# Kernel optimization log

Hardware: AMD Instinct MI355X
Metric: run time of the kernel (lower is better)

The kernel has to match this reference:

```python
import jax, jax.numpy as jnp
import numpy as np

WINDOW = 5
PAD = WINDOW // 2


def _extract_patches(x):
    # x: (B,C,H,W) -> patches (B,C,K*K,H,W) with reflect padding, matching
    # F.pad(mode='reflect') + F.unfold(window, padding=0).
    B, C, H, W = x.shape
    xp = jnp.pad(x, ((0, 0), (0, 0), (PAD, PAD), (PAD, PAD)), mode='reflect')
    patches = jnp.stack(
        [xp[:, :, i:i + H, j:j + W] for i in range(WINDOW) for j in range(WINDOW)],
        axis=2,
    )
    return patches


def setup_inputs() -> dict:
    key = jax.random.key(0)
    k1, k2, k3 = jax.random.split(key, 3)
    x = jax.random.normal(k1, (4, 32, 256, 256), dtype=jnp.float32)
    mix = jax.random.normal(k2, (1, 32, 1, 1), dtype=jnp.float32)
    beta_raw = jax.random.normal(k3, (), dtype=jnp.float32)
    return {"x": x, "mix": mix, "beta_raw": beta_raw}


def reference(x, mix, beta_raw):
    patches = _extract_patches(x)  # (B,C,25,H,W)

    # Max filter (= max_pool2d over reflect-padded input, stride 1)
    max_out = jnp.max(patches, axis=2)

    # Soft (differentiable) median filter
    beta = 5.0 + 45.0 * jax.nn.sigmoid(beta_raw)
    center = jnp.mean(patches, axis=2, keepdims=True)
    weights = jax.nn.softmax(-beta * jnp.abs(patches - center), axis=2)
    median_out = jnp.sum(weights * patches, axis=2)

    lambda_c = jax.nn.sigmoid(mix)  # (1,C,1,1)
    return lambda_c * median_out + (1.0 - lambda_c) * max_out
```

## Files before the change

### kernel.cpp

```cpp
#include <hip/hip_runtime.h>
#include <math.h>

#define HW 256
#define TW 64
#define TH 32
#define LW 68
#define LH 36

typedef float f32x2 __attribute__((ext_vector_type(2)));

__device__ __forceinline__ int reflect_idx(int i) {
    i = (i < 0) ? -i : i;
    i = (i >= HW) ? (2 * HW - 2 - i) : i;
    return i;
}

__device__ __forceinline__ float4 max4(float4 a, float4 b) {
    float4 r; r.x = fmaxf(a.x, b.x); r.y = fmaxf(a.y, b.y);
    r.z = fmaxf(a.z, b.z); r.w = fmaxf(a.w, b.w); return r;
}
__device__ __forceinline__ float4 max34(float4 a, float4 b, float4 c) {
    float4 r; r.x = fmaxf(fmaxf(a.x, b.x), c.x); r.y = fmaxf(fmaxf(a.y, b.y), c.y);
    r.z = fmaxf(fmaxf(a.z, b.z), c.z); r.w = fmaxf(fmaxf(a.w, b.w), c.w); return r;
}
__device__ __forceinline__ float4 add4(float4 a, float4 b) {
    float4 r; r.x = a.x + b.x; r.y = a.y + b.y;
    r.z = a.z + b.z; r.w = a.w + b.w; return r;
}
__device__ __forceinline__ float4 sub4(float4 a, float4 b) {
    float4 r; r.x = a.x - b.x; r.y = a.y - b.y;
    r.z = a.z - b.z; r.w = a.w - b.w; return r;
}

__device__ __forceinline__ void proc_row(
    float4 A0, float4 B0, float4 A1, float4 B1, float4 A2, float4 B2,
    float4 A3, float4 B3, float4 A4, float4 B4,
    float4 cmA, float4 cmB, float4 csA, float4 csB,
    float bp, float c04b, float inv_bp, float lam,
    float* __restrict__ orow)
{
    const float cs[8] = {csA.x,csA.y,csA.z,csA.w, csB.x,csB.y,csB.z,csB.w};
    const float cm[8] = {cmA.x,cmA.y,cmA.z,cmA.w, cmB.x,cmB.y,cmB.z,cmB.w};
    const float vv[5][8] = {
        {A0.x,A0.y,A0.z,A0.w, B0.x,B0.y,B0.z,B0.w},
        {A1.x,A1.y,A1.z,A1.w, B1.x,B1.y,B1.z,B1.w},
        {A2.x,A2.y,A2.z,A2.w, B2.x,B2.y,B2.z,B2.w},
        {A3.x,A3.y,A3.z,A3.w, B3.x,B3.y,B3.z,B3.w},
        {A4.x,A4.y,A4.z,A4.w, B4.x,B4.y,B4.z,B4.w}};

    const float t12 = cs[1] + cs[2];
    const float t34 = cs[3] + cs[4];
    const float t56 = cs[5] + cs[6];
    const float u   = t12 + t34;
    const float w_  = t34 + t56;
    const float S[4] = {cs[0] + u, u + cs[5], cs[2] + w_, w_ + cs[7]};

    const float h12 = fmaxf(cm[1], cm[2]);
    const float h34 = fmaxf(cm[3], cm[4]);
    const float h56 = fmaxf(cm[5], cm[6]);
    const float m[4] = {fmaxf(fmaxf(cm[0], h12), h34),
                        fmaxf(fmaxf(h12, h34), cm[5]),
                        fmaxf(fmaxf(cm[2], h34), h56),
                        fmaxf(fmaxf(h34, h56), cm[7])};

    const f32x2 bp2   = {bp, bp};
    const f32x2 nbm01 = {-(S[0] * c04b), -(S[1] * c04b)};
    const f32x2 nbm23 = {-(S[2] * c04b), -(S[3] * c04b)};
    f32x2 ws01 = {0.0f, 0.0f}, ws23 = {0.0f, 0.0f};
    f32x2 wa01 = {0.0f, 0.0f}, wa23 = {0.0f, 0.0f};

    #pragma unroll
    for (int k = 0; k < 5; ++k) {
        #pragma unroll
        for (int j = 0; j < 5; ++j) {
            const f32x2 v01 = {vv[k][j],     vv[k][j + 1]};
            const f32x2 v23 = {vv[k][j + 2], vv[k][j + 3]};
            const f32x2 tv01 = __builtin_elementwise_fma(bp2, v01, nbm01);
            const f32x2 tv23 = __builtin_elementwise_fma(bp2, v23, nbm23);
            f32x2 e01, e23;
            e01.x = __builtin_amdgcn_exp2f(-fabsf(tv01.x));
            e01.y = __builtin_amdgcn_exp2f(-fabsf(tv01.y));
            e23.x = __builtin_amdgcn_exp2f(-fabsf(tv23.x));
            e23.y = __builtin_amdgcn_exp2f(-fabsf(tv23.y));
            ws01 += e01;
            ws23 += e23;
            wa01 = __builtin_elementwise_fma(e01, tv01, wa01);
            wa23 = __builtin_elementwise_fma(e23, tv23, wa23);
        }
    }

    const float ws[4] = {ws01.x, ws01.y, ws23.x, ws23.y};
    const float wa[4] = {wa01.x, wa01.y, wa23.x, wa23.y};

    float o[4];
    #pragma unroll
    for (int p = 0; p < 4; ++p) {
        const float mean = S[p] * 0.04f;
        const float med  = fmaf(wa[p] * __builtin_amdgcn_rcpf(ws[p]), inv_bp, mean);
        o[p] = fmaf(lam, med - m[p], m[p]);
    }
    float4 o4; o4.x = o[0]; o4.y = o[1]; o4.z = o[2]; o4.w = o[3];
    *(float4*)orow = o4;
}

__global__ __launch_bounds__(256, 4)
void maxmedian_kernel(const float* __restrict__ x,
                      const float* __restrict__ mix,
                      const float* __restrict__ beta_raw,
                      float* __restrict__ out,
                      int C) {
    __shared__ __align__(16) float tile[LH * LW];

    const int tiles_x = HW / TW;
    const int tiles_per_plane = tiles_x * (HW / TH);
    const int plane = blockIdx.x / tiles_per_plane;
    const int t     = blockIdx.x % tiles_per_plane;
    const int ty0 = (t / tiles_x) * TH;
    const int tx0 = (t % tiles_x) * TW;

    const float* __restrict__ xp = x + (size_t)plane * (HW * HW);
    const int tid = threadIdx.x;

    {
        const int c   = tid & 63;
        const int r0s = tid >> 6;
        const int gx  = tx0 + c;
        #pragma unroll
        for (int k = 0; k < 9; ++k) {
            const int r  = r0s + 4 * k;
            const int gy = reflect_idx(ty0 + r - 2);
            tile[r * LW + c + 2] = xp[gy * HW + gx];
        }
        if (tid < 144) {
            const int jj = tid & 3;
            const int j  = (jj < 2) ? jj : (64 + jj);
            const int r  = tid >> 2;
            const int gx2 = reflect_idx(tx0 + j - 2);
            const int gy2 = reflect_idx(ty0 + r - 2);
            tile[r * LW + j] = xp[gy2 * HW + gx2];
        }
    }
    __syncthreads();

    const int ch = plane % C;
    const float lam  = 1.0f / (1.0f + __expf(-mix[ch]));
    const float beta = 5.0f + 45.0f / (1.0f + __expf(-beta_raw[0]));
    const float bp     = beta * 1.44269504088896f;
    const float inv_bp = 1.0f / bp;
    const float c04b   = 0.04f * bp;

    const int tx  = tid & 15;
    const int ryq = tid >> 4;
    const int r0  = ryq * 2;
    const float* lbase = &tile[r0 * LW + 4 * tx];

    float4 w0a = *(const float4*)(lbase + 0 * LW);
    float4 w0b = *(const float4*)(lbase + 0 * LW + 4);
    float4 w1a = *(const float4*)(lbase + 1 * LW);
    float4 w1b = *(const float4*)(lbase + 1 * LW + 4);
    float4 w2a = *(const float4*)(lbase + 2 * LW);
    float4 w2b = *(const float4*)(lbase + 2 * LW + 4);
    float4 w3a = *(const float4*)(lbase + 3 * LW);
    float4 w3b = *(const float4*)(lbase + 3 * LW + 4);
    float4 w4a = *(const float4*)(lbase + 4 * LW);
    float4 w4b = *(const float4*)(lbase + 4 * LW + 4);
    float4 w5a = *(const float4*)(lbase + 5 * LW);
    float4 w5b = *(const float4*)(lbase + 5 * LW + 4);

    float4 csA = add4(add4(add4(w0a, w1a), add4(w2a, w3a)), w4a);
    float4 csB = add4(add4(add4(w0b, w1b), add4(w2b, w3b)), w4b);

    const float4 p12a = max4(w1a, w2a), p12b = max4(w1b, w2b);
    const float4 p34a = max4(w3a, w4a), p34b = max4(w3b, w4b);
    const float4 cm0a = max34(w0a, p12a, p34a);
    const float4 cm0b = max34(w0b, p12b, p34b);

    float* __restrict__ orow =
        out + (size_t)plane * (HW * HW) + (size_t)(ty0 + r0) * HW + (tx0 + 4 * tx);

    proc_row(w0a,w0b, w1a,w1b, w2a,w2b, w3a,w3b, w4a,w4b,
             cm0a, cm0b, csA, csB, bp, c04b, inv_bp, lam, orow);

    csA = add4(csA, sub4(w5a, w0a));
    csB = add4(csB, sub4(w5b, w0b));
    const float4 cm1a = max34(p12a, p34a, w5a);
    const float4 cm1b = max34(p12b, p34b, w5b);

    proc_row(w1a,w1b, w2a,w2b, w3a,w3b, w4a,w4b, w5a,w5b,
             cm1a, cm1b, csA, csB, bp, c04b, inv_bp, lam, orow + HW);
}

extern "C" void kernel_launch(void* const* d_in, const int* in_sizes, int n_in,
                              void* d_out, int out_size, void* d_ws, size_t ws_size,
                              hipStream_t stream) {
    const float* x        = (const float*)d_in[0];
    const float* mix      = (const float*)d_in[1];
    const float* beta_raw = (const float*)d_in[2];
    float* out            = (float*)d_out;

    const int planes = in_sizes[0] / (HW * HW);
    const int C      = in_sizes[1];
    const int tiles_per_plane = (HW / TW) * (HW / TH);
    const int grid = planes * tiles_per_plane;

    maxmedian_kernel<<<grid, 256, 0, stream>>>(x, mix, beta_raw, out, C);
}
```

Before: 39.33 us.

## Restructure into per-wave bands with double-buffered LDS software pipeline

Each wave now owns an 8-row band of one plane and walks four 64-column tiles. It prefetches the next tile's rows into registers while computing the current tile out of a double-buffered per-wave LDS region, and syncs with wave barriers only instead of block-wide __syncthreads. The aim is to overlap global load latency with the exp-heavy compute and to drop block synchronisation. In exchange the grid shrinks to planes*8 blocks (1024), halo rows are reloaded per 8-row band (12 loaded rows for 8 output rows, against 36 for 32 before), and register pressure rises from the staged tiles, with the occupancy hint removed.

```diff
diff --git a/kernel.cpp b/kernel.cpp
--- a/kernel.cpp
+++ b/kernel.cpp
@@ -2,10 +2,9 @@
 #include <math.h>
 
 #define HW 256
-#define TW 64
-#define TH 32
 #define LW 68
-#define LH 36
+#define WLH 12
+#define NT 4
 
 typedef float f32x2 __attribute__((ext_vector_type(2)));
 
@@ -31,6 +30,11 @@
     float4 r; r.x = a.x - b.x; r.y = a.y - b.y;
     r.z = a.z - b.z; r.w = a.w - b.w; return r;
 }
+
+struct Stage {
+    float m[WLH];
+    float h;
+};
 
 __device__ __forceinline__ void proc_row(
     float4 A0, float4 B0, float4 A1, float4 B1, float4 A2, float4 B2,
@@ -103,44 +107,32 @@
     *(float4*)orow = o4;
 }
 
-__global__ __launch_bounds__(256, 4)
+__global__ __launch_bounds__(256)
 void maxmedian_kernel(const float* __restrict__ x,
                       const float* __restrict__ mix,
                       const float* __restrict__ beta_raw,
                       float* __restrict__ out,
                       int C) {
-    __shared__ __align__(16) float tile[LH * LW];
-
-    const int tiles_x = HW / TW;
-    const int tiles_per_plane = tiles_x * (HW / TH);
-    const int plane = blockIdx.x / tiles_per_plane;
-    const int t     = blockIdx.x % tiles_per_plane;
-    const int ty0 = (t / tiles_x) * TH;
-    const int tx0 = (t % tiles_x) * TW;
+    __shared__ __align__(16) float lds[4][2][WLH * LW];
+
+    const int tid  = threadIdx.x;
+    const int wave = tid >> 6;
+    const int lane = tid & 63;
+
+    const int band  = blockIdx.x * 4 + wave;
+    const int plane = band >> 5;
+    const int by0   = (band & 31) << 3;
 
     const float* __restrict__ xp = x + (size_t)plane * (HW * HW);
-    const int tid = threadIdx.x;
-
-    {
-        const int c   = tid & 63;
-        const int r0s = tid >> 6;
-        const int gx  = tx0 + c;
-        #pragma unroll
-        for (int k = 0; k < 9; ++k) {
-            const int r  = r0s + 4 * k;
-            const int gy = reflect_idx(ty0 + r - 2);
-            tile[r * LW + c + 2] = xp[gy * HW + gx];
-        }
-        if (tid < 144) {
-            const int jj = tid & 3;
-            const int j  = (jj < 2) ? jj : (64 + jj);
-            const int r  = tid >> 2;
-            const int gx2 = reflect_idx(tx0 + j - 2);
-            const int gy2 = reflect_idx(ty0 + r - 2);
-            tile[r * LW + j] = xp[gy2 * HW + gx2];
-        }
-    }
-    __syncthreads();
+
+    int gy[WLH];
+    #pragma unroll
+    for (int k = 0; k < WLH; ++k) gy[k] = reflect_idx(by0 - 2 + k) * HW;
+
+    const int hj   = lane & 3;
+    const int hcol = (hj < 2) ? hj : (64 + hj);
+    const int hoff = hcol - 2;
+    const int gyh  = reflect_idx(by0 - 2 + (lane >> 2)) * HW;
 
     const int ch = plane % C;
     const float lam  = 1.0f / (1.0f + __expf(-mix[ch]));
@@ -149,45 +141,87 @@
     const float inv_bp = 1.0f / bp;
     const float c04b   = 0.04f * bp;
 
-    const int tx  = tid & 15;
-    const int ryq = tid >> 4;
-    const int r0  = ryq * 2;
-    const float* lbase = &tile[r0 * LW + 4 * tx];
-
-    float4 w0a = *(const float4*)(lbase + 0 * LW);
-    float4 w0b = *(const float4*)(lbase + 0 * LW + 4);
-    float4 w1a = *(const float4*)(lbase + 1 * LW);
-    float4 w1b = *(const float4*)(lbase + 1 * LW + 4);
-    float4 w2a = *(const float4*)(lbase + 2 * LW);
-    float4 w2b = *(const float4*)(lbase + 2 * LW + 4);
-    float4 w3a = *(const float4*)(lbase + 3 * LW);
-    float4 w3b = *(const float4*)(lbase + 3 * LW + 4);
-    float4 w4a = *(const float4*)(lbase + 4 * LW);
-    float4 w4b = *(const float4*)(lbase + 4 * LW + 4);
-    float4 w5a = *(const float4*)(lbase + 5 * LW);
-    float4 w5b = *(const float4*)(lbase + 5 * LW + 4);
-
-    float4 csA = add4(add4(add4(w0a, w1a), add4(w2a, w3a)), w4a);
-    float4 csB = add4(add4(add4(w0b, w1b), add4(w2b, w3b)), w4b);
-
-    const float4 p12a = max4(w1a, w2a), p12b = max4(w1b, w2b);
-    const float4 p34a = max4(w3a, w4a), p34b = max4(w3b, w4b);
-    const float4 cm0a = max34(w0a, p12a, p34a);
-    const float4 cm0b = max34(w0b, p12b, p34b);
-
-    float* __restrict__ orow =
-        out + (size_t)plane * (HW * HW) + (size_t)(ty0 + r0) * HW + (tx0 + 4 * tx);
-
-    proc_row(w0a,w0b, w1a,w1b, w2a,w2b, w3a,w3b, w4a,w4b,
-             cm0a, cm0b, csA, csB, bp, c04b, inv_bp, lam, orow);
-
-    csA = add4(csA, sub4(w5a, w0a));
-    csB = add4(csB, sub4(w5b, w0b));
-    const float4 cm1a = max34(p12a, p34a, w5a);
-    const float4 cm1b = max34(p12b, p34b, w5b);
-
-    proc_row(w1a,w1b, w2a,w2b, w3a,w3b, w4a,w4b, w5a,w5b,
-             cm1a, cm1b, csA, csB, bp, c04b, inv_bp, lam, orow + HW);
+    const int tx = lane & 15;
+    const int r0 = (lane >> 4) * 2;
+
+    auto stage_load = [&](int t, Stage& s) {
+        const int c0 = t * 64;
+        #pragma unroll
+        for (int k = 0; k < WLH; ++k)
+            s.m[k] = xp[gy[k] + c0 + lane];
+        if (lane < 48)
+            s.h = xp[gyh + reflect_idx(c0 + hoff)];
+    };
+    auto stage_write = [&](int buf, const Stage& s) {
+        float* __restrict__ b = lds[wave][buf];
+        #pragma unroll
+        for (int k = 0; k < WLH; ++k)
+            b[k * LW + 2 + lane] = s.m[k];
+        if (lane < 48)
+            b[(lane >> 2) * LW + hcol] = s.h;
+    };
+    auto compute = [&](int t, int buf) {
+        const float* lbase = &lds[wave][buf][r0 * LW + 4 * tx];
+
+        float4 w0a = *(const float4*)(lbase + 0 * LW);
+        float4 w0b = *(const float4*)(lbase + 0 * LW + 4);
+        float4 w1a = *(const float4*)(lbase + 1 * LW);
+        float4 w1b = *(const float4*)(lbase + 1 * LW + 4);
+        float4 w2a = *(const float4*)(lbase + 2 * LW);
+        float4 w2b = *(const float4*)(lbase + 2 * LW + 4);
+        float4 w3a = *(const float4*)(lbase + 3 * LW);
+        float4 w3b = *(const float4*)(lbase + 3 * LW + 4);
+        float4 w4a = *(const float4*)(lbase + 4 * LW);
+        float4 w4b = *(const float4*)(lbase + 4 * LW + 4);
+        float4 w5a = *(const float4*)(lbase + 5 * LW);
+        float4 w5b = *(const float4*)(lbase + 5 * LW + 4);
+
+        float4 csA = add4(add4(add4(w0a, w1a), add4(w2a, w3a)), w4a);
+        float4 csB = add4(add4(add4(w0b, w1b), add4(w2b, w3b)), w4b);
+
+        const float4 p12a = max4(w1a, w2a), p12b = max4(w1b, w2b);
+        const float4 p34a = max4(w3a, w4a), p34b = max4(w3b, w4b);
+        const float4 cm0a = max34(w0a, p12a, p34a);
+        const float4 cm0b = max34(w0b, p12b, p34b);
+
+        float* __restrict__ orow =
+            out + (size_t)plane * (HW * HW) + (size_t)(by0 + r0) * HW + (t * 64 + 4 * tx);
+
+        proc_row(w0a,w0b, w1a,w1b, w2a,w2b, w3a,w3b, w4a,w4b,
+                 cm0a, cm0b, csA, csB, bp, c04b, inv_bp, lam, orow);
+
+        csA = add4(csA, sub4(w5a, w0a));
+        csB = add4(csB, sub4(w5b, w0b));
+        const float4 cm1a = max34(p12a, p34a, w5a);
+        const float4 cm1b = max34(p12b, p34b, w5b);
+
+        proc_row(w1a,w1b, w2a,w2b, w3a,w3b, w4a,w4b, w5a,w5b,
+                 cm1a, cm1b, csA, csB, bp, c04b, inv_bp, lam, orow + HW);
+    };
+
+    float* out_ = out;  (void)out_;
+
+    Stage s0, s1, s2, s3;
+    stage_load(0, s0);
+    stage_write(0, s0);
+    __builtin_amdgcn_wave_barrier();
+
+    stage_load(1, s1);
+    compute(0, 0);
+    stage_write(1, s1);
+    __builtin_amdgcn_wave_barrier();
+
+    stage_load(2, s2);
+    compute(1, 1);
+    stage_write(0, s2);
+    __builtin_amdgcn_wave_barrier();
+
+    stage_load(3, s3);
+    compute(2, 0);
+    stage_write(1, s3);
+    __builtin_amdgcn_wave_barrier();
+
+    compute(3, 1);
 }
 
 extern "C" void kernel_launch(void* const* d_in, const int* in_sizes, int n_in,
@@ -200,8 +234,7 @@
 
     const int planes = in_sizes[0] / (HW * HW);
     const int C      = in_sizes[1];
-    const int tiles_per_plane = (HW / TW) * (HW / TH);
-    const int grid = planes * tiles_per_plane;
+    const int grid = planes * 8;
 
     maxmedian_kernel<<<grid, 256, 0, stream>>>(x, mix, beta_raw, out, C);
 }
```

Measured after the change: 37.62 us. 4.3% less time.
